# Performance work log

Hardware: AMD Instinct MI355X
Metric: run time of the kernel (lower is better)

Reference implementation:

```python
import jax, jax.numpy as jnp
import numpy as np

B, C, D = 2048, 64, 1024
K_ACTIVE = 4  # exactly 4 active channels per sample; in expected_k range [2,5]
SCORE_W, MARGIN_W, TOPK_W = 3.0, 1.0, 2.0
CONTRAST_W, SPATIAL_W, NETWORK_W = 1.0, 0.5, 0.5
MARGIN, TEMP = 0.15, 0.07
N_POS = K_ACTIVE * (K_ACTIVE - 1)                       # active-active pairs (no diag)
N_NEG_PER = (K_ACTIVE * (C - K_ACTIVE)) // N_POS        # torch .view column count = (C-K)/(K-1)
_OFFDIAG = np.where(~np.eye(K_ACTIVE, dtype=bool).reshape(-1))[0]  # static row-major off-diag idx


def setup_inputs() -> dict:
    key = jax.random.key(0)
    k1, k2, k3, k4, k5 = jax.random.split(key, 5)
    # exactly K_ACTIVE active channels per sample (sorted indices)
    act_idx = jnp.sort(jnp.argsort(jax.random.uniform(k1, (B, C)), axis=1)[:, :K_ACTIVE], axis=1)
    true_labels = jnp.zeros((B, C), jnp.int32).at[jnp.arange(B)[:, None], act_idx].set(1)
    pred_scores = jax.random.uniform(k2, (B, C), minval=0.01, maxval=0.99)  # valid BCE probs
    embeddings = jax.random.normal(k3, (B, C, D), jnp.float32)
    channel_positions = jax.random.normal(k4, (C, 3), jnp.float32)
    connectivity_matrix = jax.random.uniform(k5, (C, C), jnp.float32)
    return {"pred_scores": pred_scores, "true_labels": true_labels, "embeddings": embeddings,
            "channel_positions": channel_positions, "connectivity_matrix": connectivity_matrix}


def _total_loss(pred_scores, embeddings, channel_positions, connectivity_matrix, true_labels):
    labf = true_labels.astype(pred_scores.dtype)
    bidx = jnp.arange(B)[:, None]
    # 1) score loss: BCE(pred, labels)
    loss_score = -jnp.mean(labf * jnp.log(pred_scores) + (1.0 - labf) * jnp.log1p(-pred_scores))
    # 2) margin ranking loss (every sample has both actives and inactives by construction)
    n_act = labf.sum(1)
    n_inact = (1.0 - labf).sum(1)
    act_mean = (pred_scores * labf).sum(1) / n_act
    inact_mean = (pred_scores * (1.0 - labf)).sum(1) / n_inact
    loss_margin = jnp.mean(jax.nn.relu(MARGIN - (act_mean - inact_mean)))
    # 3) top-k IoU loss; k = max(2, min(true_k, 5)) = K_ACTIVE (static by construction)
    _, topk_idx = jax.lax.top_k(pred_scores, K_ACTIVE)
    pred_mask = jnp.zeros((B, C), bool).at[bidx, topk_idx].set(True)
    true_mask = true_labels == 1
    inter = (pred_mask & true_mask).sum(1).astype(pred_scores.dtype)
    union = (pred_mask | true_mask).sum(1).astype(pred_scores.dtype)
    loss_topk = jnp.mean(1.0 - inter / (union + 1e-8))
    # 4) contrastive loss: sorted active/inactive index sets preserve torch's row-major
    #    boolean-mask extraction order of sim_matrix[pos_mask] / sim_matrix[neg_mask]
    order = jnp.argsort(true_labels, axis=1, stable=True)  # inactive idx first, both ascending
    inact_idx = order[:, : C - K_ACTIVE]
    act_idx = order[:, C - K_ACTIVE:]
    nrm = jnp.linalg.norm(embeddings, axis=-1, keepdims=True)
    emb_norm = embeddings / jnp.maximum(nrm, 1e-12)  # F.normalize semantics
    act_emb = emb_norm[bidx, act_idx]      # (B, K, D)
    inact_emb = emb_norm[bidx, inact_idx]  # (B, C-K, D)  -- only needed sim entries computed
    sim_aa = jnp.einsum('bkd,bjd->bkj', act_emb, act_emb) / TEMP     # (B, K, K)
    sim_ai = jnp.einsum('bkd,bjd->bkj', act_emb, inact_emb) / TEMP   # (B, K, C-K)
    pos_sim = sim_aa.reshape(B, K_ACTIVE * K_ACTIVE)[:, _OFFDIAG]    # (B, N_POS)
    neg_sim = sim_ai.reshape(B, N_POS, N_NEG_PER)                    # torch .view(-1, n_neg//n_pos)
    logits = jnp.concatenate([pos_sim[:, :, None], neg_sim], axis=2) # (B, N_POS, 1+N_NEG_PER)
    ce = jax.nn.logsumexp(logits, axis=2) - logits[:, :, 0]          # cross_entropy, target=0
    loss_contrastive = jnp.mean(ce)  # mean over N_POS rows then over samples
    # 5) spatial clustering: mean pairwise distance among channels with score > 0.5
    diff = channel_positions[:, None, :] - channel_positions[None, :, :]
    d2 = jnp.sum(diff * diff, axis=-1)                     # (C, C)
    eye = jnp.eye(C, dtype=pred_scores.dtype)
    dist = jnp.sqrt(d2 + eye) * (1.0 - eye)                # grad-safe sqrt on diag, then zeroed
    m = (pred_scores > 0.5).astype(pred_scores.dtype)      # (B, C)
    n_m = m.sum(1)
    pair_sum = jnp.einsum('bi,ij,bj->b', m, dist, m)       # each unordered pair counted twice
    avg_dist = jnp.where(n_m >= 2.0, pair_sum / jnp.maximum(n_m * (n_m - 1.0), 1.0), 0.0)
    loss_spatial = jnp.mean(avg_dist)                      # torch divides by batch incl. skipped
    # 6) network coherence: -mean(scores^T W scores / C^2)
    coh = jnp.einsum('bi,ij,bj->b', pred_scores, connectivity_matrix, pred_scores) / (C * C)
    loss_network = jnp.mean(-coh)
    return (SCORE_W * loss_score + MARGIN_W * loss_margin + TOPK_W * loss_topk
            + CONTRAST_W * loss_contrastive + SPATIAL_W * loss_spatial + NETWORK_W * loss_network)


def reference(pred_scores, true_labels, embeddings, channel_positions, connectivity_matrix):
    return _total_loss(pred_scores, embeddings, channel_positions, connectivity_matrix, true_labels)
```

## Files before the change

kernel.cpp:

```cpp
#include <hip/hip_runtime.h>

#define B_N 2048
#define C_N 64
#define D_N 1024
#define MARGIN_C 0.15f
#define INV_TEMP (1.0f / 0.07f)

typedef float v4f __attribute__((ext_vector_type(4)));

__device__ __forceinline__ float wred(float v) {
#pragma unroll
    for (int off = 32; off > 0; off >>= 1) v += __shfl_xor(v, off, 64);
    return v;
}

__device__ __forceinline__ v4f nt_load4(const v4f* p) {
    return __builtin_nontemporal_load(p);
}

__global__ __launch_bounds__(256, 4)
void loss_kernel(const float* __restrict__ pred,
                 const int*   __restrict__ lab,
                 const float* __restrict__ emb,
                 const float* __restrict__ cpos,
                 const float* __restrict__ conn,
                 float* __restrict__ partial)
{
    __shared__ v4f   s_frag4[1024];
    __shared__ float s_p[64];
    __shared__ int   s_inact[60];
    __shared__ float s_dots[64][4];
    __shared__ float s_nsq[64];
    __shared__ float s_pos[192];
    __shared__ float s_part[6];

    const int tid  = threadIdx.x;
    const int w    = tid >> 6;
    const int lane = tid & 63;
    const int b    = blockIdx.x;

    const float p_lane = pred[b * 64 + lane];
    const int   l_lane = lab[b * 64 + lane];
    if (tid >= 64 && tid < 256) s_pos[tid - 64] = cpos[tid - 64];

    const unsigned long long mask = __ballot(l_lane != 0);
    unsigned long long mtmp = mask;
    int act[4];
#pragma unroll
    for (int j = 0; j < 4; j++) { act[j] = __builtin_ctzll(mtmp); mtmp &= mtmp - 1; }

    const v4f* base = (const v4f*)emb + (long)b * 64 * 256;
#pragma unroll
    for (int k = 0; k < 4; k++) s_frag4[k * 256 + tid] = base[act[k] * 256 + tid];

    if (w == 0) {
        s_p[lane] = p_lane;
        if (!((mask >> lane) & 1ull)) {
            int r = __popcll(~mask & ((1ull << lane) - 1ull));
            s_inact[r] = lane;
        }
    }
    __syncthreads();

    v4f frag[4][4];
#pragma unroll
    for (int j = 0; j < 4; j++)
#pragma unroll
        for (int t = 0; t < 4; t++) frag[j][t] = s_frag4[j * 256 + lane + 64 * t];

    auto compute_row = [&](const v4f* buf, int c) {
        float a0 = 0.f, a1 = 0.f, a2 = 0.f, a3 = 0.f, ns = 0.f;
#pragma unroll
        for (int t = 0; t < 4; t++) {
            v4f u = buf[t];
            ns += u.x * u.x + u.y * u.y + u.z * u.z + u.w * u.w;
            a0 += u.x * frag[0][t].x + u.y * frag[0][t].y + u.z * frag[0][t].z + u.w * frag[0][t].w;
            a1 += u.x * frag[1][t].x + u.y * frag[1][t].y + u.z * frag[1][t].z + u.w * frag[1][t].w;
            a2 += u.x * frag[2][t].x + u.y * frag[2][t].y + u.z * frag[2][t].z + u.w * frag[2][t].w;
            a3 += u.x * frag[3][t].x + u.y * frag[3][t].y + u.z * frag[3][t].z + u.w * frag[3][t].w;
        }
#pragma unroll
        for (int off = 32; off > 0; off >>= 1) {
            a0 += __shfl_xor(a0, off, 64); a1 += __shfl_xor(a1, off, 64);
            a2 += __shfl_xor(a2, off, 64); a3 += __shfl_xor(a3, off, 64);
            ns += __shfl_xor(ns, off, 64);
        }
        if (lane == 0) {
            s_dots[c][0] = a0; s_dots[c][1] = a1; s_dots[c][2] = a2; s_dots[c][3] = a3;
            s_nsq[c] = ns;
        }
    };

    const v4f* wbase = base + (w * 16) * 256;
    v4f bufA[4], bufB[4];
#pragma unroll
    for (int t = 0; t < 4; t++) bufA[t] = nt_load4(wbase + lane + 64 * t);

#pragma unroll 1
    for (int i = 0; i < 16; i += 2) {
        const int c0 = w * 16 + i;
        {
            const v4f* s = wbase + (i + 1) * 256;
#pragma unroll
            for (int t = 0; t < 4; t++) bufB[t] = nt_load4(s + lane + 64 * t);
        }
        compute_row(bufA, c0);
        if (i < 14) {
            const v4f* s = wbase + (i + 2) * 256;
#pragma unroll
            for (int t = 0; t < 4; t++) bufA[t] = nt_load4(s + lane + 64 * t);
        }
        compute_row(bufB, c0 + 1);
    }
    __syncthreads();

    if (w == 0) {
        float ce = 0.0f;
        if (lane < 12) {
            int k = lane / 3;
            int r = lane % 3;
            int m = r + ((r >= k) ? 1 : 0);
            float nk = fmaxf(sqrtf(s_nsq[act[k]]), 1e-12f);
            float nm = fmaxf(sqrtf(s_nsq[act[m]]), 1e-12f);
            float posv = s_dots[act[k]][m] / (nk * nm) * INV_TEMP;
            float neg[20];
            float mx = posv;
            int base2 = r * 20;
#pragma unroll
            for (int t = 0; t < 20; t++) {
                int c = s_inact[base2 + t];
                float nc = fmaxf(sqrtf(s_nsq[c]), 1e-12f);
                neg[t] = s_dots[c][k] / (nk * nc) * INV_TEMP;
                mx = fmaxf(mx, neg[t]);
            }
            float sum = __expf(posv - mx);
#pragma unroll
            for (int t = 0; t < 20; t++) sum += __expf(neg[t] - mx);
            ce = logf(sum) + mx - posv;
        }
        ce = wred(ce);
        if (lane == 0) s_part[0] = ce;
    } else if (w == 1) {
        float sc = l_lane ? -logf(p_lane) : -log1pf(-p_lane);
        sc = wred(sc);
        float s1 = wred(l_lane ? p_lane : 0.0f);
        float s2 = wred(p_lane);
        float pv = p_lane;
        int inter = 0;
#pragma unroll
        for (int it = 0; it < 4; it++) {
            float v = pv;
            int   ix = lane;
#pragma unroll
            for (int off = 32; off > 0; off >>= 1) {
                float ov = __shfl_xor(v, off, 64);
                int   oi = __shfl_xor(ix, off, 64);
                if (ov > v || (ov == v && oi < ix)) { v = ov; ix = oi; }
            }
            if (lane == ix) pv = -1e30f;
            if ((mask >> ix) & 1ull) inter++;
        }
        if (lane == 0) {
            s_part[1] = sc;
            float am = s1 * (1.0f / 4.0f);
            float im = (s2 - s1) * (1.0f / 60.0f);
            s_part[2] = fmaxf(MARGIN_C - (am - im), 0.0f);
            float fi = (float)inter;
            float un = (float)(8 - inter);
            s_part[3] = 1.0f - fi / (un + 1e-8f);
        }
    } else if (w == 2) {
        bool  mj = p_lane > 0.5f;
        float px = s_pos[lane * 3 + 0];
        float py = s_pos[lane * 3 + 1];
        float pz = s_pos[lane * 3 + 2];
        float tj = 0.0f;
        for (int i = 0; i < 64; i++) {
            float dx = s_pos[i * 3 + 0] - px;
            float dy = s_pos[i * 3 + 1] - py;
            float dz = s_pos[i * 3 + 2] - pz;
            float d2 = dx * dx + dy * dy + dz * dz;
            bool on = (i != lane) && (s_p[i] > 0.5f);
            tj += on ? sqrtf(d2) : 0.0f;
        }
        float pair = wred(mj ? tj : 0.0f);
        unsigned long long bal = __ballot(mj);
        int nm = __popcll(bal);
        if (lane == 0) {
            s_part[4] = (nm >= 2) ? pair / fmaxf((float)nm * (float)(nm - 1), 1.0f) : 0.0f;
        }
    } else {
        float tj = 0.0f;
        for (int i = 0; i < 64; i++) tj += s_p[i] * conn[i * 64 + lane];
        float coh = wred(tj * p_lane);
        if (lane == 0) s_part[5] = -coh * (1.0f / 4096.0f);
    }
    __syncthreads();

    if (tid == 0) {
        partial[b] = 3.0f * s_part[1] * (1.0f / 64.0f)
                   + s_part[2]
                   + 2.0f * s_part[3]
                   + s_part[0] * (1.0f / 12.0f)
                   + 0.5f * s_part[4]
                   + 0.5f * s_part[5];
    }
}

__global__ void finalize_kernel(const float* __restrict__ partial, float* __restrict__ out) {
    __shared__ float sm[4];
    const int tid  = threadIdx.x;
    const int w    = tid >> 6;
    const int lane = tid & 63;
    float s = 0.0f;
    for (int i = tid; i < B_N; i += 256) s += partial[i];
    s = wred(s);
    if (lane == 0) sm[w] = s;
    __syncthreads();
    if (tid == 0) out[0] = (sm[0] + sm[1] + sm[2] + sm[3]) * (1.0f / (float)B_N);
}

extern "C" void kernel_launch(void* const* d_in, const int* in_sizes, int n_in,
                              void* d_out, int out_size, void* d_ws, size_t ws_size,
                              hipStream_t stream) {
    const float* pred = (const float*)d_in[0];
    const int*   lab  = (const int*)d_in[1];
    const float* emb  = (const float*)d_in[2];
    const float* cpos = (const float*)d_in[3];
    const float* conn = (const float*)d_in[4];
    float* out = (float*)d_out;
    float* partial = (float*)d_ws;

    loss_kernel<<<B_N, 256, 0, stream>>>(pred, lab, emb, cpos, conn, partial);
    finalize_kernel<<<1, 256, 0, stream>>>(partial, out);
}
```

Before: 678.3 us.

## Prefetch first rows early, reuse active rows, overlap scalar losses, merge shuffle reductions

The first two embedding rows per wave are now loaded before the label/pred setup, so global latency overlaps the prologue. The scalar losses (BCE, margin, top-k, spatial, network) now run before the dot-product loop rather than after it. Rows that are active channels are taken from registers instead of being reloaded from global memory. The five per-row butterfly reductions are merged into a transpose-style reduction with fewer shuffles, and the dots and norms share one LDS array. Register pressure rises from holding both prefetch buffers early, and the kernel is bound by streaming 512MB of embeddings.

```diff
diff --git a/kernel.cpp b/kernel.cpp
--- a/kernel.cpp
+++ b/kernel.cpp
@@ -29,8 +29,7 @@
     __shared__ v4f   s_frag4[1024];
     __shared__ float s_p[64];
     __shared__ int   s_inact[60];
-    __shared__ float s_dots[64][4];
-    __shared__ float s_nsq[64];
+    __shared__ float s_dn[64][5];
     __shared__ float s_pos[192];
     __shared__ float s_part[6];
 
@@ -38,6 +37,15 @@
     const int w    = tid >> 6;
     const int lane = tid & 63;
     const int b    = blockIdx.x;
+    const int w16  = w * 16;
+
+    const v4f* base = (const v4f*)emb + (long)b * 64 * 256;
+
+    v4f bufA[4], bufB[4];
+#pragma unroll
+    for (int t = 0; t < 4; t++) bufA[t] = nt_load4(base + (w16 + 0) * 256 + lane + 64 * t);
+#pragma unroll
+    for (int t = 0; t < 4; t++) bufB[t] = nt_load4(base + (w16 + 1) * 256 + lane + 64 * t);
 
     const float p_lane = pred[b * 64 + lane];
     const int   l_lane = lab[b * 64 + lane];
@@ -49,7 +57,6 @@
 #pragma unroll
     for (int j = 0; j < 4; j++) { act[j] = __builtin_ctzll(mtmp); mtmp &= mtmp - 1; }
 
-    const v4f* base = (const v4f*)emb + (long)b * 64 * 256;
 #pragma unroll
     for (int k = 0; k < 4; k++) s_frag4[k * 256 + tid] = base[act[k] * 256 + tid];
 
@@ -62,85 +69,7 @@
     }
     __syncthreads();
 
-    v4f frag[4][4];
-#pragma unroll
-    for (int j = 0; j < 4; j++)
-#pragma unroll
-        for (int t = 0; t < 4; t++) frag[j][t] = s_frag4[j * 256 + lane + 64 * t];
-
-    auto compute_row = [&](const v4f* buf, int c) {
-        float a0 = 0.f, a1 = 0.f, a2 = 0.f, a3 = 0.f, ns = 0.f;
-#pragma unroll
-        for (int t = 0; t < 4; t++) {
-            v4f u = buf[t];
-            ns += u.x * u.x + u.y * u.y + u.z * u.z + u.w * u.w;
-            a0 += u.x * frag[0][t].x + u.y * frag[0][t].y + u.z * frag[0][t].z + u.w * frag[0][t].w;
-            a1 += u.x * frag[1][t].x + u.y * frag[1][t].y + u.z * frag[1][t].z + u.w * frag[1][t].w;
-            a2 += u.x * frag[2][t].x + u.y * frag[2][t].y + u.z * frag[2][t].z + u.w * frag[2][t].w;
-            a3 += u.x * frag[3][t].x + u.y * frag[3][t].y + u.z * frag[3][t].z + u.w * frag[3][t].w;
-        }
-#pragma unroll
-        for (int off = 32; off > 0; off >>= 1) {
-            a0 += __shfl_xor(a0, off, 64); a1 += __shfl_xor(a1, off, 64);
-            a2 += __shfl_xor(a2, off, 64); a3 += __shfl_xor(a3, off, 64);
-            ns += __shfl_xor(ns, off, 64);
-        }
-        if (lane == 0) {
-            s_dots[c][0] = a0; s_dots[c][1] = a1; s_dots[c][2] = a2; s_dots[c][3] = a3;
-            s_nsq[c] = ns;
-        }
-    };
-
-    const v4f* wbase = base + (w * 16) * 256;
-    v4f bufA[4], bufB[4];
-#pragma unroll
-    for (int t = 0; t < 4; t++) bufA[t] = nt_load4(wbase + lane + 64 * t);
-
-#pragma unroll 1
-    for (int i = 0; i < 16; i += 2) {
-        const int c0 = w * 16 + i;
-        {
-            const v4f* s = wbase + (i + 1) * 256;
-#pragma unroll
-            for (int t = 0; t < 4; t++) bufB[t] = nt_load4(s + lane + 64 * t);
-        }
-        compute_row(bufA, c0);
-        if (i < 14) {
-            const v4f* s = wbase + (i + 2) * 256;
-#pragma unroll
-            for (int t = 0; t < 4; t++) bufA[t] = nt_load4(s + lane + 64 * t);
-        }
-        compute_row(bufB, c0 + 1);
-    }
-    __syncthreads();
-
-    if (w == 0) {
-        float ce = 0.0f;
-        if (lane < 12) {
-            int k = lane / 3;
-            int r = lane % 3;
-            int m = r + ((r >= k) ? 1 : 0);
-            float nk = fmaxf(sqrtf(s_nsq[act[k]]), 1e-12f);
-            float nm = fmaxf(sqrtf(s_nsq[act[m]]), 1e-12f);
-            float posv = s_dots[act[k]][m] / (nk * nm) * INV_TEMP;
-            float neg[20];
-            float mx = posv;
-            int base2 = r * 20;
-#pragma unroll
-            for (int t = 0; t < 20; t++) {
-                int c = s_inact[base2 + t];
-                float nc = fmaxf(sqrtf(s_nsq[c]), 1e-12f);
-                neg[t] = s_dots[c][k] / (nk * nc) * INV_TEMP;
-                mx = fmaxf(mx, neg[t]);
-            }
-            float sum = __expf(posv - mx);
-#pragma unroll
-            for (int t = 0; t < 20; t++) sum += __expf(neg[t] - mx);
-            ce = logf(sum) + mx - posv;
-        }
-        ce = wred(ce);
-        if (lane == 0) s_part[0] = ce;
-    } else if (w == 1) {
+    if (w == 1) {
         float sc = l_lane ? -logf(p_lane) : -log1pf(-p_lane);
         sc = wred(sc);
         float s1 = wred(l_lane ? p_lane : 0.0f);
@@ -189,11 +118,115 @@
         if (lane == 0) {
             s_part[4] = (nm >= 2) ? pair / fmaxf((float)nm * (float)(nm - 1), 1.0f) : 0.0f;
         }
-    } else {
+    } else if (w == 3) {
         float tj = 0.0f;
         for (int i = 0; i < 64; i++) tj += s_p[i] * conn[i * 64 + lane];
         float coh = wred(tj * p_lane);
         if (lane == 0) s_part[5] = -coh * (1.0f / 4096.0f);
+    }
+
+    v4f frag[4][4];
+#pragma unroll
+    for (int j = 0; j < 4; j++)
+#pragma unroll
+        for (int t = 0; t < 4; t++) frag[j][t] = s_frag4[j * 256 + lane + 64 * t];
+
+    auto compute_row = [&](const v4f* buf, int c) {
+        float a0 = 0.f, a1 = 0.f, a2 = 0.f, a3 = 0.f, ns = 0.f;
+#pragma unroll
+        for (int t = 0; t < 4; t++) {
+            v4f u = buf[t];
+            ns += u.x * u.x + u.y * u.y + u.z * u.z + u.w * u.w;
+            a0 += u.x * frag[0][t].x + u.y * frag[0][t].y + u.z * frag[0][t].z + u.w * frag[0][t].w;
+            a1 += u.x * frag[1][t].x + u.y * frag[1][t].y + u.z * frag[1][t].z + u.w * frag[1][t].w;
+            a2 += u.x * frag[2][t].x + u.y * frag[2][t].y + u.z * frag[2][t].z + u.w * frag[2][t].w;
+            a3 += u.x * frag[3][t].x + u.y * frag[3][t].y + u.z * frag[3][t].z + u.w * frag[3][t].w;
+        }
+        const bool hi32 = (lane & 32) != 0;
+        float u01 = hi32 ? a1 : a0;
+        float v01 = hi32 ? a0 : a1;
+        u01 += __shfl_xor(v01, 32, 64);
+        float u23 = hi32 ? a3 : a2;
+        float v23 = hi32 ? a2 : a3;
+        u23 += __shfl_xor(v23, 32, 64);
+        ns  += __shfl_xor(ns, 32, 64);
+
+        const bool hi16 = (lane & 16) != 0;
+        float x = hi16 ? u23 : u01;
+        float y = hi16 ? u01 : u23;
+        x  += __shfl_xor(y, 16, 64);
+        ns += __shfl_xor(ns, 16, 64);
+
+        const bool hi8 = (lane & 8) != 0;
+        float z  = hi8 ? ns : x;
+        float zz = hi8 ? x : ns;
+        z += __shfl_xor(zz, 8, 64);
+
+        z += __shfl_xor(z, 4, 64);
+        z += __shfl_xor(z, 2, 64);
+        z += __shfl_xor(z, 1, 64);
+        if ((lane & 7) == 0) {
+            int g = lane >> 3;
+            int slot = (g == 1) ? 4 : ((g & 2) | (g >> 2));
+            if (!(g & 1) || g == 1) s_dn[c][slot] = z;
+        }
+    };
+
+    auto fill_row = [&](v4f* buf, int c) {
+        if (c == act[0]) {
+#pragma unroll
+            for (int t = 0; t < 4; t++) buf[t] = frag[0][t];
+        } else if (c == act[1]) {
+#pragma unroll
+            for (int t = 0; t < 4; t++) buf[t] = frag[1][t];
+        } else if (c == act[2]) {
+#pragma unroll
+            for (int t = 0; t < 4; t++) buf[t] = frag[2][t];
+        } else if (c == act[3]) {
+#pragma unroll
+            for (int t = 0; t < 4; t++) buf[t] = frag[3][t];
+        } else {
+#pragma unroll
+            for (int t = 0; t < 4; t++) buf[t] = nt_load4(base + c * 256 + lane + 64 * t);
+        }
+    };
+
+#pragma unroll 1
+    for (int i = 0; i < 16; i += 2) {
+        const int c0 = w16 + i;
+        compute_row(bufA, c0);
+        if (i < 14) fill_row(bufA, c0 + 2);
+        compute_row(bufB, c0 + 1);
+        if (i < 14) fill_row(bufB, c0 + 3);
+    }
+    __syncthreads();
+
+    if (w == 0) {
+        float ce = 0.0f;
+        if (lane < 12) {
+            int k = lane / 3;
+            int r = lane % 3;
+            int m = r + ((r >= k) ? 1 : 0);
+            float nk = fmaxf(sqrtf(s_dn[act[k]][4]), 1e-12f);
+            float nm = fmaxf(sqrtf(s_dn[act[m]][4]), 1e-12f);
+            float posv = s_dn[act[k]][m] / (nk * nm) * INV_TEMP;
+            float neg[20];
+            float mx = posv;
+            int base2 = r * 20;
+#pragma unroll
+            for (int t = 0; t < 20; t++) {
+                int c = s_inact[base2 + t];
+                float nc = fmaxf(sqrtf(s_dn[c][4]), 1e-12f);
+                neg[t] = s_dn[c][k] / (nk * nc) * INV_TEMP;
+                mx = fmaxf(mx, neg[t]);
+            }
+            float sum = __expf(posv - mx);
+#pragma unroll
+            for (int t = 0; t < 20; t++) sum += __expf(neg[t] - mx);
+            ce = logf(sum) + mx - posv;
+        }
+        ce = wred(ce);
+        if (lane == 0) s_part[0] = ce;
     }
     __syncthreads();
 
```

Result: no change. 688.8 us (+1.5%).
